# Optimization experiments

Measured on AMD Instinct MI355X. Metric: run time of the kernel, lower is better.

Reference implementation:

```python
import jax, jax.numpy as jnp
import numpy as np

NUM_EXPERTS = 64
TOP_K = 8
HIDDEN = 2048
MLP = 768
TOKENS = 1024


def setup_inputs() -> dict:
    key = jax.random.key(0)
    ks = jax.random.split(key, 5)
    hidden_states = jax.random.normal(ks[0], (TOKENS, HIDDEN), dtype=jnp.float32)
    # lecun-normal-ish scaling (std = 1/sqrt(fan_in))
    router_w = jax.random.normal(ks[1], (HIDDEN, NUM_EXPERTS), dtype=jnp.float32) / np.sqrt(HIDDEN)
    gate_proj = jax.random.normal(ks[2], (NUM_EXPERTS, HIDDEN, MLP), dtype=jnp.float32) / np.sqrt(HIDDEN)
    up_proj = jax.random.normal(ks[3], (NUM_EXPERTS, HIDDEN, MLP), dtype=jnp.float32) / np.sqrt(HIDDEN)
    down_proj = jax.random.normal(ks[4], (NUM_EXPERTS, MLP, HIDDEN), dtype=jnp.float32) / np.sqrt(MLP)
    return {
        "hidden_states": hidden_states,
        "router_w": router_w,
        "gate_proj": gate_proj,
        "up_proj": up_proj,
        "down_proj": down_proj,
    }


def reference(hidden_states, router_w, gate_proj, up_proj, down_proj):
    # Router: [T, E]
    router_logits = hidden_states @ router_w
    # Top-k routing, softmax renormalized over the selected k (norm_topk_prob=True)
    routing_weights, selected_experts = jax.lax.top_k(router_logits, k=TOP_K)
    routing_weights = jax.nn.softmax(routing_weights, axis=-1)  # [T, k]

    sel_flat = selected_experts.ravel()  # [T*k] int32
    # Duplicate each token for each of its k experts: [T*k, H]
    x_exp = jnp.repeat(hidden_states, TOP_K, axis=0)

    # prepare_routing: sort token copies by expert id, count per-expert group sizes
    sort_idx = jnp.argsort(sel_flat)          # stable sort of expert ids
    x_sorted = x_exp[sort_idx]                # [T*k, H] grouped by expert
    group_sizes = jnp.zeros((NUM_EXPERTS,), dtype=jnp.int32).at[sel_flat].add(1)
    unsort_idx = jnp.argsort(sort_idx)

    # Grouped GEMMs (megablox-style) via ragged_dot
    gate_out = jax.lax.ragged_dot(x_sorted, gate_proj, group_sizes)   # [T*k, M]
    up_out = jax.lax.ragged_dot(x_sorted, up_proj, group_sizes)       # [T*k, M]
    down_out = jax.lax.ragged_dot(jax.nn.silu(gate_out) * up_out, down_proj, group_sizes)  # [T*k, H]

    # Unsort back to (token, k) order and combine with routing weights
    unsorted = down_out[unsort_idx].reshape(-1, TOP_K, HIDDEN)
    return jnp.sum(unsorted * routing_weights[..., None], axis=1)  # [T, H]
```

## Files before the change

kernel.cpp:

```cpp
#include <hip/hip_runtime.h>
#include <hip/hip_bf16.h>

#define T_TOKENS 1024
#define HID      2048
#define NEXP     64
#define TOPK     8
#define MLP      768
#define NPAIR    (T_TOKENS * TOPK)

typedef __bf16 bf16x8 __attribute__((ext_vector_type(8)));
typedef float  f32x4  __attribute__((ext_vector_type(4)));
typedef unsigned int u32x2 __attribute__((ext_vector_type(2)));
typedef unsigned int u32x4 __attribute__((ext_vector_type(4)));

#define LDK 40

static __device__ __forceinline__ unsigned short f2bf(float f) {
    __hip_bfloat16 h = __float2bfloat16(f);
    unsigned short u;
    __builtin_memcpy(&u, &h, sizeof(u));
    return u;
}
static __device__ __forceinline__ unsigned int pk2bf(float a, float b) {
    return (unsigned int)f2bf(a) | ((unsigned int)f2bf(b) << 16);
}

__global__ __launch_bounds__(256) void router_topk_kernel(
    const float* __restrict__ hs, const float* __restrict__ rw,
    int* __restrict__ sel, float* __restrict__ wts, unsigned short* __restrict__ xb)
{
    const int lane = threadIdx.x & 63;
    const int tg   = threadIdx.x >> 6;
    const int t    = blockIdx.x * 4 + tg;

    {
        const float* xr = hs + (size_t)t * HID;
        unsigned short* xw = xb + (size_t)t * HID;
        #pragma unroll
        for (int c = 0; c < 4; ++c) {
            int i = (lane + c * 64) * 8;
            f32x4 a = *(const f32x4*)(xr + i);
            f32x4 b = *(const f32x4*)(xr + i + 4);
            u32x4 v;
            v[0] = pk2bf(a[0], a[1]); v[1] = pk2bf(a[2], a[3]);
            v[2] = pk2bf(b[0], b[1]); v[3] = pk2bf(b[2], b[3]);
            *(u32x4*)(xw + i) = v;
        }
    }

    const float4* x4 = (const float4*)(hs + (size_t)t * HID);
    float acc = 0.f;
    for (int h4 = 0; h4 < HID / 4; ++h4) {
        float4 xv = x4[h4];
        int hb = h4 * 4 * NEXP + lane;
        acc += xv.x * rw[hb] + xv.y * rw[hb + NEXP]
             + xv.z * rw[hb + 2 * NEXP] + xv.w * rw[hb + 3 * NEXP];
    }

    float v = acc;
    float tv[TOPK]; int ti[TOPK];
    for (int i = 0; i < TOPK; ++i) {
        float m = v; int mi = lane;
        for (int off = 32; off > 0; off >>= 1) {
            float om  = __shfl_xor(m, off, 64);
            int   omi = __shfl_xor(mi, off, 64);
            if (om > m || (om == m && omi < mi)) { m = om; mi = omi; }
        }
        tv[i] = m; ti[i] = mi;
        if (lane == mi) v = -__builtin_inff();
    }
    if (lane == 0) {
        float mx = tv[0], s = 0.f, e[TOPK];
        for (int i = 0; i < TOPK; ++i) { e[i] = __expf(tv[i] - mx); s += e[i]; }
        float inv = 1.f / s;
        for (int i = 0; i < TOPK; ++i) {
            wts[t * TOPK + i] = e[i] * inv;
            sel[t * TOPK + i] = ti[i];
        }
    }
}

__global__ __launch_bounds__(1024) void route_kernel(
    const int* __restrict__ sel, int* __restrict__ offsets, int* __restrict__ rows)
{
    __shared__ int cnt[NEXP];
    __shared__ int cur[NEXP];
    const int t = threadIdx.x;
    if (t < NEXP) cnt[t] = 0;
    __syncthreads();
    int e[8];
    const int p0 = t * 8;
    #pragma unroll
    for (int j = 0; j < 8; ++j) {
        e[j] = sel[p0 + j];
        atomicAdd(&cnt[e[j]], 1);
    }
    __syncthreads();
    if (t == 0) {
        int s = 0;
        for (int i = 0; i < NEXP; ++i) { cur[i] = s; offsets[i] = s; s += cnt[i]; }
        offsets[NEXP] = s;
    }
    __syncthreads();
    #pragma unroll
    for (int j = 0; j < 8; ++j) {
        int pos = atomicAdd(&cur[e[j]], 1);
        rows[pos] = p0 + j;
    }
}

__global__ __launch_bounds__(256, 2) void gateup_kernel(
    const unsigned short* __restrict__ xb, const float* __restrict__ gw,
    const float* __restrict__ uw, const int* __restrict__ offsets,
    const int* __restrict__ rows, unsigned short* __restrict__ hb)
{
    const int bid = blockIdx.x;
    const int sw  = (bid & 7) * 96 + (bid >> 3);
    const int e   = sw / 12;
    const int n0  = (sw % 12) * 64;

    const int r0 = offsets[e];
    const int nrows = offsets[e + 1] - r0;
    if (nrows <= 0) return;

    __shared__ __align__(16) float smemf[12800];
    unsigned short* smem = (unsigned short*)smemf;

    const int thr  = threadIdx.x;
    const int wave = thr >> 6;
    const int lane = thr & 63;
    const int wg   = wave & 1;
    const int isUp = wave >> 1;
    const int fr   = lane & 15;
    const int fq   = lane >> 4;
    const int mofs_c = isUp ? 10240 : 7680;

    const int ar = thr >> 2;
    const int ac = (thr & 3) * 8;

    const int tt   = thr & 127;
    const int wk2  = tt & 15;
    const int nst  = (tt >> 4) * 8;
    const float* wsrc = (thr >= 128 ? uw : gw)
        + (size_t)e * HID * MLP + (size_t)(2 * wk2) * MLP + n0 + nst;
    const int mofs_s = (thr >= 128) ? 10240 : 7680;

    const int NS = HID / 32;

    for (int m0 = 0; m0 < nrows; m0 += 192) {
        const unsigned short *ap0, *ap1, *ap2;
        bool av0, av1, av2;
        {
            int gr0 = m0 + ar, gr1 = m0 + ar + 64, gr2 = m0 + ar + 128;
            av0 = gr0 < nrows; av1 = gr1 < nrows; av2 = gr2 < nrows;
            int p0 = av0 ? rows[r0 + gr0] : 0;
            int p1 = av1 ? rows[r0 + gr1] : 0;
            int p2 = av2 ? rows[r0 + gr2] : 0;
            ap0 = xb + (size_t)(p0 >> 3) * HID + ac;
            ap1 = xb + (size_t)(p1 >> 3) * HID + ac;
            ap2 = xb + (size_t)(p2 >> 3) * HID + ac;
        }

        u32x4 va0, va1, va2;
        f32x4 wAe, wBe, wCe, wDe, wAo, wBo, wCo, wDo;
        const u32x4 uz = (u32x4){0u, 0u, 0u, 0u};
        const f32x4 fz = (f32x4){0.f, 0.f, 0.f, 0.f};

        auto LOAD_A = [&](int s) {
            va0 = av0 ? *(const u32x4*)(ap0 + s * 32) : uz;
            va1 = av1 ? *(const u32x4*)(ap1 + s * 32) : uz;
            va2 = av2 ? *(const u32x4*)(ap2 + s * 32) : uz;
        };
        auto WRITE_A = [&](int s) {
            unsigned short* b = smem + (s & 1) * 12800;
            *(u32x4*)(b + ar * LDK + ac) = va0;
            *(u32x4*)(b + (ar + 64) * LDK + ac) = va1;
            *(u32x4*)(b + (ar + 128) * LDK + ac) = va2;
        };
        auto LOAD_WE = [&](int s) {
            const float* wp = wsrc + (size_t)s * 32 * MLP;
            wAe = *(const f32x4*)wp;        wBe = *(const f32x4*)(wp + 4);
            wCe = *(const f32x4*)(wp + MLP); wDe = *(const f32x4*)(wp + MLP + 4);
        };
        auto LOAD_WO = [&](int s) {
            const float* wp = wsrc + (size_t)s * 32 * MLP;
            wAo = *(const f32x4*)wp;        wBo = *(const f32x4*)(wp + 4);
            wCo = *(const f32x4*)(wp + MLP); wDo = *(const f32x4*)(wp + MLP + 4);
        };
        auto WRITE_WE = [&](int s) {
            unsigned short* wb = smem + (s & 1) * 12800 + mofs_s;
            #pragma unroll
            for (int j = 0; j < 4; ++j) {
                *(unsigned int*)(wb + (nst + j) * LDK + 2 * wk2)     = pk2bf(wAe[j], wCe[j]);
                *(unsigned int*)(wb + (nst + 4 + j) * LDK + 2 * wk2) = pk2bf(wBe[j], wDe[j]);
            }
        };
        auto WRITE_WO = [&](int s) {
            unsigned short* wb = smem + (s & 1) * 12800 + mofs_s;
            #pragma unroll
            for (int j = 0; j < 4; ++j) {
                *(unsigned int*)(wb + (nst + j) * LDK + 2 * wk2)     = pk2bf(wAo[j], wCo[j]);
                *(unsigned int*)(wb + (nst + 4 + j) * LDK + 2 * wk2) = pk2bf(wBo[j], wDo[j]);
            }
        };

        f32x4 acc[6][4];
        #pragma unroll
        for (int ms = 0; ms < 6; ++ms)
            #pragma unroll
            for (int ns = 0; ns < 4; ++ns) acc[ms][ns] = fz;

        const int rem = nrows - m0 - wg * 96;

        auto STEP = [&](const unsigned short* bb) {
            const unsigned short* wbb = bb + mofs_c;
            bf16x8 wF0 = *(const bf16x8*)(wbb + (0 * 16 + fr) * LDK + fq * 8);
            bf16x8 wF1 = *(const bf16x8*)(wbb + (1 * 16 + fr) * LDK + fq * 8);
            bf16x8 wF2 = *(const bf16x8*)(wbb + (2 * 16 + fr) * LDK + fq * 8);
            bf16x8 wF3 = *(const bf16x8*)(wbb + (3 * 16 + fr) * LDK + fq * 8);
            bf16x8 aF[6];
            #pragma unroll
            for (int ms = 0; ms < 6; ++ms)
                aF[ms] = *(const bf16x8*)(bb + (wg * 96 + ms * 16 + fr) * LDK + fq * 8);
            #pragma unroll
            for (int ms = 0; ms < 6; ++ms) {
                if (rem > ms * 16) {
                    acc[ms][0] = __builtin_amdgcn_mfma_f32_16x16x32_bf16(aF[ms], wF0, acc[ms][0], 0, 0, 0);
                    acc[ms][1] = __builtin_amdgcn_mfma_f32_16x16x32_bf16(aF[ms], wF1, acc[ms][1], 0, 0, 0);
                    acc[ms][2] = __builtin_amdgcn_mfma_f32_16x16x32_bf16(aF[ms], wF2, acc[ms][2], 0, 0, 0);
                    acc[ms][3] = __builtin_amdgcn_mfma_f32_16x16x32_bf16(aF[ms], wF3, acc[ms][3], 0, 0, 0);
                }
            }
        };

        LOAD_WE(0);
        LOAD_WO(1);
        LOAD_A(0);
        WRITE_WE(0);
        WRITE_A(0);
        LOAD_A(1);
        asm volatile("s_waitcnt lgkmcnt(0)" ::: "memory");
        __builtin_amdgcn_s_barrier();

        for (int s = 0; s < NS; s += 2) {
            if (s + 2 < NS) LOAD_WE(s + 2);
            STEP(smem);
            WRITE_WO(s + 1);
            WRITE_A(s + 1);
            if (s + 2 < NS) LOAD_A(s + 2);
            asm volatile("s_waitcnt lgkmcnt(0)" ::: "memory");
            __builtin_amdgcn_s_barrier();
            if (s + 3 < NS) LOAD_WO(s + 3);
            STEP(smem + 12800);
            if (s + 2 < NS) { WRITE_WE(s + 2); WRITE_A(s + 2); }
            if (s + 3 < NS) LOAD_A(s + 3);
            asm volatile("s_waitcnt lgkmcnt(0)" ::: "memory");
            __builtin_amdgcn_s_barrier();
        }

        float* xbf = smemf;
        if (isUp) {
            #pragma unroll
            for (int ms = 0; ms < 6; ++ms)
                #pragma unroll
                for (int i = 0; i < 4; ++i) {
                    int lrow = wg * 96 + ms * 16 + fq * 4 + i;
                    #pragma unroll
                    for (int ns = 0; ns < 4; ++ns)
                        xbf[lrow * 65 + ns * 16 + fr] = acc[ms][ns][i];
                }
        }
        __syncthreads();
        if (!isUp) {
            #pragma unroll
            for (int ms = 0; ms < 6; ++ms)
                #pragma unroll
                for (int i = 0; i < 4; ++i) {
                    int lrow = wg * 96 + ms * 16 + fq * 4 + i;
                    int grow = m0 + lrow;
                    if (grow < nrows) {
                        unsigned short* drow = hb + (size_t)(r0 + grow) * MLP + n0;
                        #pragma unroll
                        for (int ns = 0; ns < 4; ++ns) {
                            float g = acc[ms][ns][i];
                            float u = xbf[lrow * 65 + ns * 16 + fr];
                            float h = g * u / (1.f + __expf(-g));
                            drow[ns * 16 + fr] = f2bf(h);
                        }
                    }
                }
        }
        __syncthreads();
    }
}

__global__ __launch_bounds__(256, 2) void down_kernel(
    const unsigned short* __restrict__ hb, const float* __restrict__ dw,
    const int* __restrict__ offsets, const int* __restrict__ rows,
    const float* __restrict__ wts, float* __restrict__ out)
{
    const int bid = blockIdx.x;
    const int sw  = (bid & 7) * 128 + (bid >> 3);
    const int e   = sw >> 4;
    const int n0  = (sw & 15) * 128;

    const int r0 = offsets[e];
    const int nrows = offsets[e + 1] - r0;
    if (nrows <= 0) return;

    __shared__ __align__(16) float smemf[12800];
    unsigned short* smem = (unsigned short*)smemf;

    const int thr  = threadIdx.x;
    const int wave = thr >> 6;
    const int lane = thr & 63;
    const int wg   = wave & 1;
    const int wn   = wave >> 1;
    const int fr   = lane & 15;
    const int fq   = lane >> 4;

    const int ar = thr >> 2;
    const int ac = (thr & 3) * 8;

    const int wk2 = thr & 15;
    const int nst = (thr >> 4) * 8;
    const float* wsrc = dw + (size_t)e * MLP * HID + (size_t)(2 * wk2) * HID + n0 + nst;

    const int NS = MLP / 32;

    for (int m0 = 0; m0 < nrows; m0 += 192) {
        const bool av0 = (m0 + ar)       < nrows;
        const bool av1 = (m0 + ar + 64)  < nrows;
        const bool av2 = (m0 + ar + 128) < nrows;
        const unsigned short* hp0 = hb + (size_t)(r0 + m0 + ar) * MLP + ac;
        const unsigned short* hp1 = hp0 + (size_t)64  * MLP;
        const unsigned short* hp2 = hp0 + (size_t)128 * MLP;

        u32x4 ua0, ua1, ua2;
        f32x4 wAe, wBe, wCe, wDe, wAo, wBo, wCo, wDo;
        const u32x4 uz = (u32x4){0u, 0u, 0u, 0u};
        const f32x4 fz = (f32x4){0.f, 0.f, 0.f, 0.f};

        auto LOAD_A = [&](int s) {
            ua0 = av0 ? *(const u32x4*)(hp0 + s * 32) : uz;
            ua1 = av1 ? *(const u32x4*)(hp1 + s * 32) : uz;
            ua2 = av2 ? *(const u32x4*)(hp2 + s * 32) : uz;
        };
        auto WRITE_A = [&](int s) {
            unsigned short* b = smem + (s & 1) * 12800;
            *(u32x4*)(b + ar * LDK + ac) = ua0;
            *(u32x4*)(b + (ar + 64) * LDK + ac) = ua1;
            *(u32x4*)(b + (ar + 128) * LDK + ac) = ua2;
        };
        auto LOAD_WE = [&](int s) {
            const float* wp = wsrc + (size_t)s * 32 * HID;
            wAe = *(const f32x4*)wp;        wBe = *(const f32x4*)(wp + 4);
            wCe = *(const f32x4*)(wp + HID); wDe = *(const f32x4*)(wp + HID + 4);
        };
        auto LOAD_WO = [&](int s) {
            const float* wp = wsrc + (size_t)s * 32 * HID;
            wAo = *(const f32x4*)wp;        wBo = *(const f32x4*)(wp + 4);
            wCo = *(const f32x4*)(wp + HID); wDo = *(const f32x4*)(wp + HID + 4);
        };
        auto WRITE_WE = [&](int s) {
            unsigned short* wb = smem + (s & 1) * 12800 + 7680;
            #pragma unroll
            for (int j = 0; j < 4; ++j) {
                *(unsigned int*)(wb + (nst + j) * LDK + 2 * wk2)     = pk2bf(wAe[j], wCe[j]);
                *(unsigned int*)(wb + (nst + 4 + j) * LDK + 2 * wk2) = pk2bf(wBe[j], wDe[j]);
            }
        };
        auto WRITE_WO = [&](int s) {
            unsigned short* wb = smem + (s & 1) * 12800 + 7680;
            #pragma unroll
            for (int j = 0; j < 4; ++j) {
                *(unsigned int*)(wb + (nst + j) * LDK + 2 * wk2)     = pk2bf(wAo[j], wCo[j]);
                *(unsigned int*)(wb + (nst + 4 + j) * LDK + 2 * wk2) = pk2bf(wBo[j], wDo[j]);
            }
        };

        f32x4 acc[6][4];
        #pragma unroll
        for (int ms = 0; ms < 6; ++ms)
            #pragma unroll
            for (int ns = 0; ns < 4; ++ns) acc[ms][ns] = fz;

        const int rem = nrows - m0 - wg * 96;

        auto STEP = [&](const unsigned short* bb) {
            const unsigned short* wbb = bb + 7680;
            bf16x8 wF0 = *(const bf16x8*)(wbb + (wn * 64 + 0 * 16 + fr) * LDK + fq * 8);
            bf16x8 wF1 = *(const bf16x8*)(wbb + (wn * 64 + 1 * 16 + fr) * LDK + fq * 8);
            bf16x8 wF2 = *(const bf16x8*)(wbb + (wn * 64 + 2 * 16 + fr) * LDK + fq * 8);
            bf16x8 wF3 = *(const bf16x8*)(wbb + (wn * 64 + 3 * 16 + fr) * LDK + fq * 8);
            bf16x8 aF[6];
            #pragma unroll
            for (int ms = 0; ms < 6; ++ms)
                aF[ms] = *(const bf16x8*)(bb + (wg * 96 + ms * 16 + fr) * LDK + fq * 8);
            #pragma unroll
            for (int ms = 0; ms < 6; ++ms) {
                if (rem > ms * 16) {
                    acc[ms][0] = __builtin_amdgcn_mfma_f32_16x16x32_bf16(aF[ms], wF0, acc[ms][0], 0, 0, 0);
                    acc[ms][1] = __builtin_amdgcn_mfma_f32_16x16x32_bf16(aF[ms], wF1, acc[ms][1], 0, 0, 0);
                    acc[ms][2] = __builtin_amdgcn_mfma_f32_16x16x32_bf16(aF[ms], wF2, acc[ms][2], 0, 0, 0);
                    acc[ms][3] = __builtin_amdgcn_mfma_f32_16x16x32_bf16(aF[ms], wF3, acc[ms][3], 0, 0, 0);
                }
            }
        };

        LOAD_WE(0);
        LOAD_WO(1);
        LOAD_A(0);
        WRITE_WE(0);
        WRITE_A(0);
        LOAD_A(1);
        asm volatile("s_waitcnt lgkmcnt(0)" ::: "memory");
        __builtin_amdgcn_s_barrier();

        for (int s = 0; s < NS; s += 2) {
            if (s + 2 < NS) LOAD_WE(s + 2);
            STEP(smem);
            WRITE_WO(s + 1);
            WRITE_A(s + 1);
            if (s + 2 < NS) LOAD_A(s + 2);
            asm volatile("s_waitcnt lgkmcnt(0)" ::: "memory");
            __builtin_amdgcn_s_barrier();
            if (s + 3 < NS) LOAD_WO(s + 3);
            STEP(smem + 12800);
            if (s + 2 < NS) { WRITE_WE(s + 2); WRITE_A(s + 2); }
            if (s + 3 < NS) LOAD_A(s + 3);
            asm volatile("s_waitcnt lgkmcnt(0)" ::: "memory");
            __builtin_amdgcn_s_barrier();
        }

        #pragma unroll
        for (int ms = 0; ms < 6; ++ms) {
            #pragma unroll
            for (int i = 0; i < 4; ++i) {
                int lrow = wg * 96 + ms * 16 + fq * 4 + i;
                int grow = m0 + lrow;
                if (grow < nrows) {
                    int p  = rows[r0 + grow];
                    float w = wts[p];
                    float* orow = out + (size_t)(p >> 3) * HID + n0 + wn * 64;
                    #pragma unroll
                    for (int ns = 0; ns < 4; ++ns)
                        atomicAdd(orow + ns * 16 + fr, acc[ms][ns][i] * w);
                }
            }
        }
        __syncthreads();
    }
}

extern "C" void kernel_launch(void* const* d_in, const int* in_sizes, int n_in,
                              void* d_out, int out_size, void* d_ws, size_t ws_size,
                              hipStream_t stream)
{
    const float* hs = (const float*)d_in[0];
    const float* rw = (const float*)d_in[1];
    const float* gw = (const float*)d_in[2];
    const float* uw = (const float*)d_in[3];
    const float* dw = (const float*)d_in[4];
    float* out = (float*)d_out;

    char* ws = (char*)d_ws;
    int*   sel     = (int*)(ws);
    float* wts     = (float*)(ws + 32768);
    int*   offsets = (int*)(ws + 65792);
    int*   rows    = (int*)(ws + 66560);
    unsigned short* xb = (unsigned short*)(ws + 99328);
    unsigned short* hb = (unsigned short*)(ws + 99328 + 4194304);

    hipMemsetAsync(out, 0, (size_t)T_TOKENS * HID * sizeof(float), stream);

    router_topk_kernel<<<T_TOKENS / 4, 256, 0, stream>>>(hs, rw, sel, wts, xb);
    route_kernel<<<1, 1024, 0, stream>>>(sel, offsets, rows);
    gateup_kernel<<<768, 256, 0, stream>>>(xb, gw, uw, offsets, rows, hb);
    down_kernel<<<1024, 256, 0, stream>>>(hb, dw, offsets, rows, wts, out);
}
```

Measured before the change: 1.198 ms.

## Use 512-thread gate/up blocks and replace atomic scatter with per-pair buffer plus combine

The gate/up kernel moves to 512 threads (8 waves), each wave covering 48 rows instead of 96, which halves per-wave accumulator registers and spreads the global loads across more threads. The down kernel becomes a template that, when the workspace is large enough, writes unweighted per-pair outputs to a scratch buffer. A separate combine kernel then sums the top-k pairs per token with the routing weights. This drops the output memset and the float atomics, but adds a 64 MB intermediate write and read, and the old atomic path remains as a fallback.

Result: faster. 1.163 ms, median of 3 (-2.9%).

```diff
diff --git a/kernel.cpp b/kernel.cpp
--- a/kernel.cpp
+++ b/kernel.cpp
@@ -109,7 +109,7 @@
     }
 }
 
-__global__ __launch_bounds__(256, 2) void gateup_kernel(
+__global__ __launch_bounds__(512) void gateup_kernel(
     const unsigned short* __restrict__ xb, const float* __restrict__ gw,
     const float* __restrict__ uw, const int* __restrict__ offsets,
     const int* __restrict__ rows, unsigned short* __restrict__ hb)
@@ -129,21 +129,19 @@
     const int thr  = threadIdx.x;
     const int wave = thr >> 6;
     const int lane = thr & 63;
-    const int wg   = wave & 1;
-    const int isUp = wave >> 1;
+    const int wg   = wave & 3;
+    const int isUp = wave >> 2;
     const int fr   = lane & 15;
     const int fq   = lane >> 4;
-    const int mofs_c = isUp ? 10240 : 7680;
-
-    const int ar = thr >> 2;
-    const int ac = (thr & 3) * 8;
-
-    const int tt   = thr & 127;
-    const int wk2  = tt & 15;
-    const int nst  = (tt >> 4) * 8;
-    const float* wsrc = (thr >= 128 ? uw : gw)
-        + (size_t)e * HID * MLP + (size_t)(2 * wk2) * MLP + n0 + nst;
-    const int mofs_s = (thr >= 128) ? 10240 : 7680;
+
+    const int ar = thr >> 3;
+    const int ac = (thr & 7) * 4;
+
+    const int wk2 = thr & 15;
+    const int wnq = (thr & 255) >> 4;
+    const float* wsrc = (thr >= 256 ? uw : gw)
+        + (size_t)e * HID * MLP + (size_t)(2 * wk2) * MLP + n0 + wnq * 4;
+    const int mofs = (thr >= 256) ? 10240 : 7680;
 
     const int NS = HID / 32;
 
@@ -161,34 +159,215 @@
             ap2 = xb + (size_t)(p2 >> 3) * HID + ac;
         }
 
-        u32x4 va0, va1, va2;
+        u32x2 va0, va1, va2;
+        f32x4 w0e, w1e, w0o, w1o;
+        const u32x2 z2 = (u32x2){0u, 0u};
+        const f32x4 fz = (f32x4){0.f, 0.f, 0.f, 0.f};
+
+        auto LOAD_A = [&](int s) {
+            va0 = av0 ? *(const u32x2*)(ap0 + s * 32) : z2;
+            va1 = av1 ? *(const u32x2*)(ap1 + s * 32) : z2;
+            va2 = av2 ? *(const u32x2*)(ap2 + s * 32) : z2;
+        };
+        auto WRITE_A = [&](int s) {
+            unsigned short* b = smem + (s & 1) * 12800;
+            *(u32x2*)(b + ar * LDK + ac) = va0;
+            *(u32x2*)(b + (ar + 64) * LDK + ac) = va1;
+            *(u32x2*)(b + (ar + 128) * LDK + ac) = va2;
+        };
+        auto LOAD_WE = [&](int s) {
+            const float* wp = wsrc + (size_t)s * 32 * MLP;
+            w0e = *(const f32x4*)wp;  w1e = *(const f32x4*)(wp + MLP);
+        };
+        auto LOAD_WO = [&](int s) {
+            const float* wp = wsrc + (size_t)s * 32 * MLP;
+            w0o = *(const f32x4*)wp;  w1o = *(const f32x4*)(wp + MLP);
+        };
+        auto WRITE_WE = [&](int s) {
+            unsigned short* wb = smem + (s & 1) * 12800 + mofs;
+            #pragma unroll
+            for (int i = 0; i < 4; ++i)
+                *(unsigned int*)(wb + (wnq * 4 + i) * LDK + 2 * wk2) = pk2bf(w0e[i], w1e[i]);
+        };
+        auto WRITE_WO = [&](int s) {
+            unsigned short* wb = smem + (s & 1) * 12800 + mofs;
+            #pragma unroll
+            for (int i = 0; i < 4; ++i)
+                *(unsigned int*)(wb + (wnq * 4 + i) * LDK + 2 * wk2) = pk2bf(w0o[i], w1o[i]);
+        };
+
+        f32x4 acc[3][4];
+        #pragma unroll
+        for (int ms = 0; ms < 3; ++ms)
+            #pragma unroll
+            for (int ns = 0; ns < 4; ++ns) acc[ms][ns] = fz;
+
+        const int rem = nrows - m0 - wg * 48;
+
+        LOAD_WE(0);
+        LOAD_WO(1);
+        LOAD_A(0);
+        WRITE_WE(0);
+        WRITE_A(0);
+        LOAD_A(1);
+        asm volatile("s_waitcnt lgkmcnt(0)" ::: "memory");
+        __builtin_amdgcn_s_barrier();
+
+        #define GU_MFMA(BB)                                                          \
+        {                                                                            \
+            const unsigned short* wbb = (BB) + mofs;                                 \
+            bf16x8 aF0, aF1, aF2, wF0, wF1, wF2, wF3;                                \
+            wF0 = *(const bf16x8*)(wbb + (0 * 16 + fr) * LDK + fq * 8);              \
+            wF1 = *(const bf16x8*)(wbb + (1 * 16 + fr) * LDK + fq * 8);              \
+            wF2 = *(const bf16x8*)(wbb + (2 * 16 + fr) * LDK + fq * 8);              \
+            wF3 = *(const bf16x8*)(wbb + (3 * 16 + fr) * LDK + fq * 8);              \
+            aF0 = *(const bf16x8*)((BB) + (wg * 48 + fr) * LDK + fq * 8);            \
+            aF1 = *(const bf16x8*)((BB) + (wg * 48 + 16 + fr) * LDK + fq * 8);       \
+            aF2 = *(const bf16x8*)((BB) + (wg * 48 + 32 + fr) * LDK + fq * 8);       \
+            if (rem > 0) {                                                           \
+                acc[0][0] = __builtin_amdgcn_mfma_f32_16x16x32_bf16(aF0, wF0, acc[0][0], 0, 0, 0); \
+                acc[0][1] = __builtin_amdgcn_mfma_f32_16x16x32_bf16(aF0, wF1, acc[0][1], 0, 0, 0); \
+                acc[0][2] = __builtin_amdgcn_mfma_f32_16x16x32_bf16(aF0, wF2, acc[0][2], 0, 0, 0); \
+                acc[0][3] = __builtin_amdgcn_mfma_f32_16x16x32_bf16(aF0, wF3, acc[0][3], 0, 0, 0); \
+            }                                                                        \
+            if (rem > 16) {                                                          \
+                acc[1][0] = __builtin_amdgcn_mfma_f32_16x16x32_bf16(aF1, wF0, acc[1][0], 0, 0, 0); \
+                acc[1][1] = __builtin_amdgcn_mfma_f32_16x16x32_bf16(aF1, wF1, acc[1][1], 0, 0, 0); \
+                acc[1][2] = __builtin_amdgcn_mfma_f32_16x16x32_bf16(aF1, wF2, acc[1][2], 0, 0, 0); \
+                acc[1][3] = __builtin_amdgcn_mfma_f32_16x16x32_bf16(aF1, wF3, acc[1][3], 0, 0, 0); \
+            }                                                                        \
+            if (rem > 32) {                                                          \
+                acc[2][0] = __builtin_amdgcn_mfma_f32_16x16x32_bf16(aF2, wF0, acc[2][0], 0, 0, 0); \
+                acc[2][1] = __builtin_amdgcn_mfma_f32_16x16x32_bf16(aF2, wF1, acc[2][1], 0, 0, 0); \
+                acc[2][2] = __builtin_amdgcn_mfma_f32_16x16x32_bf16(aF2, wF2, acc[2][2], 0, 0, 0); \
+                acc[2][3] = __builtin_amdgcn_mfma_f32_16x16x32_bf16(aF2, wF3, acc[2][3], 0, 0, 0); \
+            }                                                                        \
+        }
+
+        for (int s = 0; s < NS; s += 2) {
+            if (s + 2 < NS) LOAD_WE(s + 2);
+            GU_MFMA(smem)
+            WRITE_WO(s + 1);
+            WRITE_A(s + 1);
+            if (s + 2 < NS) LOAD_A(s + 2);
+            asm volatile("s_waitcnt lgkmcnt(0)" ::: "memory");
+            __builtin_amdgcn_s_barrier();
+            if (s + 3 < NS) LOAD_WO(s + 3);
+            GU_MFMA(smem + 12800)
+            if (s + 2 < NS) { WRITE_WE(s + 2); WRITE_A(s + 2); }
+            if (s + 3 < NS) LOAD_A(s + 3);
+            asm volatile("s_waitcnt lgkmcnt(0)" ::: "memory");
+            __builtin_amdgcn_s_barrier();
+        }
+        #undef GU_MFMA
+
+        float* xbf = smemf;
+        if (isUp) {
+            #pragma unroll
+            for (int ms = 0; ms < 3; ++ms)
+                #pragma unroll
+                for (int i = 0; i < 4; ++i) {
+                    int lrow = wg * 48 + ms * 16 + fq * 4 + i;
+                    #pragma unroll
+                    for (int ns = 0; ns < 4; ++ns)
+                        xbf[lrow * 65 + ns * 16 + fr] = acc[ms][ns][i];
+                }
+        }
+        __syncthreads();
+        if (!isUp) {
+            #pragma unroll
+            for (int ms = 0; ms < 3; ++ms)
+                #pragma unroll
+                for (int i = 0; i < 4; ++i) {
+                    int lrow = wg * 48 + ms * 16 + fq * 4 + i;
+                    int grow = m0 + lrow;
+                    if (grow < nrows) {
+                        unsigned short* drow = hb + (size_t)(r0 + grow) * MLP + n0;
+                        #pragma unroll
+                        for (int ns = 0; ns < 4; ++ns) {
+                            float g = acc[ms][ns][i];
+                            float u = xbf[lrow * 65 + ns * 16 + fr];
+                            float h = g * u / (1.f + __expf(-g));
+                            drow[ns * 16 + fr] = f2bf(h);
+                        }
+                    }
+                }
+        }
+        __syncthreads();
+    }
+}
+
+template <int USE_ATOMIC>
+__global__ __launch_bounds__(256, 2) void down_kernel_t(
+    const unsigned short* __restrict__ hb, const float* __restrict__ dw,
+    const int* __restrict__ offsets, const int* __restrict__ rows,
+    const float* __restrict__ wts, float* __restrict__ outp)
+{
+    const int bid = blockIdx.x;
+    const int sw  = (bid & 7) * 128 + (bid >> 3);
+    const int e   = sw >> 4;
+    const int n0  = (sw & 15) * 128;
+
+    const int r0 = offsets[e];
+    const int nrows = offsets[e + 1] - r0;
+    if (nrows <= 0) return;
+
+    __shared__ __align__(16) float smemf[12800];
+    unsigned short* smem = (unsigned short*)smemf;
+
+    const int thr  = threadIdx.x;
+    const int wave = thr >> 6;
+    const int lane = thr & 63;
+    const int wg   = wave & 1;
+    const int wn   = wave >> 1;
+    const int fr   = lane & 15;
+    const int fq   = lane >> 4;
+
+    const int ar = thr >> 2;
+    const int ac = (thr & 3) * 8;
+
+    const int wk2 = thr & 15;
+    const int nst = (thr >> 4) * 8;
+    const float* wsrc = dw + (size_t)e * MLP * HID + (size_t)(2 * wk2) * HID + n0 + nst;
+
+    const int NS = MLP / 32;
+
+    for (int m0 = 0; m0 < nrows; m0 += 192) {
+        const bool av0 = (m0 + ar)       < nrows;
+        const bool av1 = (m0 + ar + 64)  < nrows;
+        const bool av2 = (m0 + ar + 128) < nrows;
+        const unsigned short* hp0 = hb + (size_t)(r0 + m0 + ar) * MLP + ac;
+        const unsigned short* hp1 = hp0 + (size_t)64  * MLP;
+        const unsigned short* hp2 = hp0 + (size_t)128 * MLP;
+
+        u32x4 ua0, ua1, ua2;
         f32x4 wAe, wBe, wCe, wDe, wAo, wBo, wCo, wDo;
         const u32x4 uz = (u32x4){0u, 0u, 0u, 0u};
         const f32x4 fz = (f32x4){0.f, 0.f, 0.f, 0.f};
 
         auto LOAD_A = [&](int s) {
-            va0 = av0 ? *(const u32x4*)(ap0 + s * 32) : uz;
-            va1 = av1 ? *(const u32x4*)(ap1 + s * 32) : uz;
-            va2 = av2 ? *(const u32x4*)(ap2 + s * 32) : uz;
+            ua0 = av0 ? *(const u32x4*)(hp0 + s * 32) : uz;
+            ua1 = av1 ? *(const u32x4*)(hp1 + s * 32) : uz;
+            ua2 = av2 ? *(const u32x4*)(hp2 + s * 32) : uz;
         };
         auto WRITE_A = [&](int s) {
             unsigned short* b = smem + (s & 1) * 12800;
-            *(u32x4*)(b + ar * LDK + ac) = va0;
-            *(u32x4*)(b + (ar + 64) * LDK + ac) = va1;
-            *(u32x4*)(b + (ar + 128) * LDK + ac) = va2;
+            *(u32x4*)(b + ar * LDK + ac) = ua0;
+            *(u32x4*)(b + (ar + 64) * LDK + ac) = ua1;
+            *(u32x4*)(b + (ar + 128) * LDK + ac) = ua2;
         };
         auto LOAD_WE = [&](int s) {
-            const float* wp = wsrc + (size_t)s * 32 * MLP;
+            const float* wp = wsrc + (size_t)s * 32 * HID;
             wAe = *(const f32x4*)wp;        wBe = *(const f32x4*)(wp + 4);
-            wCe = *(const f32x4*)(wp + MLP); wDe = *(const f32x4*)(wp + MLP + 4);
+            wCe = *(const f32x4*)(wp + HID); wDe = *(const f32x4*)(wp + HID + 4);
         };
         auto LOAD_WO = [&](int s) {
-            const float* wp = wsrc + (size_t)s * 32 * MLP;
+            const float* wp = wsrc + (size_t)s * 32 * HID;
             wAo = *(const f32x4*)wp;        wBo = *(const f32x4*)(wp + 4);
-            wCo = *(const f32x4*)(wp + MLP); wDo = *(const f32x4*)(wp + MLP + 4);
+            wCo = *(const f32x4*)(wp + HID); wDo = *(const f32x4*)(wp + HID + 4);
         };
         auto WRITE_WE = [&](int s) {
-            unsigned short* wb = smem + (s & 1) * 12800 + mofs_s;
+            unsigned short* wb = smem + (s & 1) * 12800 + 7680;
             #pragma unroll
             for (int j = 0; j < 4; ++j) {
                 *(unsigned int*)(wb + (nst + j) * LDK + 2 * wk2)     = pk2bf(wAe[j], wCe[j]);
@@ -196,7 +375,7 @@
             }
         };
         auto WRITE_WO = [&](int s) {
-            unsigned short* wb = smem + (s & 1) * 12800 + mofs_s;
+            unsigned short* wb = smem + (s & 1) * 12800 + 7680;
             #pragma unroll
             for (int j = 0; j < 4; ++j) {
                 *(unsigned int*)(wb + (nst + j) * LDK + 2 * wk2)     = pk2bf(wAo[j], wCo[j]);
@@ -213,11 +392,11 @@
         const int rem = nrows - m0 - wg * 96;
 
         auto STEP = [&](const unsigned short* bb) {
-            const unsigned short* wbb = bb + mofs_c;
-            bf16x8 wF0 = *(const bf16x8*)(wbb + (0 * 16 + fr) * LDK + fq * 8);
-            bf16x8 wF1 = *(const bf16x8*)(wbb + (1 * 16 + fr) * LDK + fq * 8);
-            bf16x8 wF2 = *(const bf16x8*)(wbb + (2 * 16 + fr) * LDK + fq * 8);
-            bf16x8 wF3 = *(const bf16x8*)(wbb + (3 * 16 + fr) * LDK + fq * 8);
+            const unsigned short* wbb = bb + 7680;
+            bf16x8 wF0 = *(const bf16x8*)(wbb + (wn * 64 + 0 * 16 + fr) * LDK + fq * 8);
+            bf16x8 wF1 = *(const bf16x8*)(wbb + (wn * 64 + 1 * 16 + fr) * LDK + fq * 8);
+            bf16x8 wF2 = *(const bf16x8*)(wbb + (wn * 64 + 2 * 16 + fr) * LDK + fq * 8);
+            bf16x8 wF3 = *(const bf16x8*)(wbb + (wn * 64 + 3 * 16 + fr) * LDK + fq * 8);
             bf16x8 aF[6];
             #pragma unroll
             for (int ms = 0; ms < 6; ++ms)
@@ -258,181 +437,6 @@
             __builtin_amdgcn_s_barrier();
         }
 
-        float* xbf = smemf;
-        if (isUp) {
-            #pragma unroll
-            for (int ms = 0; ms < 6; ++ms)
-                #pragma unroll
-                for (int i = 0; i < 4; ++i) {
-                    int lrow = wg * 96 + ms * 16 + fq * 4 + i;
-                    #pragma unroll
-                    for (int ns = 0; ns < 4; ++ns)
-                        xbf[lrow * 65 + ns * 16 + fr] = acc[ms][ns][i];
-                }
-        }
-        __syncthreads();
-        if (!isUp) {
-            #pragma unroll
-            for (int ms = 0; ms < 6; ++ms)
-                #pragma unroll
-                for (int i = 0; i < 4; ++i) {
-                    int lrow = wg * 96 + ms * 16 + fq * 4 + i;
-                    int grow = m0 + lrow;
-                    if (grow < nrows) {
-                        unsigned short* drow = hb + (size_t)(r0 + grow) * MLP + n0;
-                        #pragma unroll
-                        for (int ns = 0; ns < 4; ++ns) {
-                            float g = acc[ms][ns][i];
-                            float u = xbf[lrow * 65 + ns * 16 + fr];
-                            float h = g * u / (1.f + __expf(-g));
-                            drow[ns * 16 + fr] = f2bf(h);
-                        }
-                    }
-                }
-        }
-        __syncthreads();
-    }
-}
-
-__global__ __launch_bounds__(256, 2) void down_kernel(
-    const unsigned short* __restrict__ hb, const float* __restrict__ dw,
-    const int* __restrict__ offsets, const int* __restrict__ rows,
-    const float* __restrict__ wts, float* __restrict__ out)
-{
-    const int bid = blockIdx.x;
-    const int sw  = (bid & 7) * 128 + (bid >> 3);
-    const int e   = sw >> 4;
-    const int n0  = (sw & 15) * 128;
-
-    const int r0 = offsets[e];
-    const int nrows = offsets[e + 1] - r0;
-    if (nrows <= 0) return;
-
-    __shared__ __align__(16) float smemf[12800];
-    unsigned short* smem = (unsigned short*)smemf;
-
-    const int thr  = threadIdx.x;
-    const int wave = thr >> 6;
-    const int lane = thr & 63;
-    const int wg   = wave & 1;
-    const int wn   = wave >> 1;
-    const int fr   = lane & 15;
-    const int fq   = lane >> 4;
-
-    const int ar = thr >> 2;
-    const int ac = (thr & 3) * 8;
-
-    const int wk2 = thr & 15;
-    const int nst = (thr >> 4) * 8;
-    const float* wsrc = dw + (size_t)e * MLP * HID + (size_t)(2 * wk2) * HID + n0 + nst;
-
-    const int NS = MLP / 32;
-
-    for (int m0 = 0; m0 < nrows; m0 += 192) {
-        const bool av0 = (m0 + ar)       < nrows;
-        const bool av1 = (m0 + ar + 64)  < nrows;
-        const bool av2 = (m0 + ar + 128) < nrows;
-        const unsigned short* hp0 = hb + (size_t)(r0 + m0 + ar) * MLP + ac;
-        const unsigned short* hp1 = hp0 + (size_t)64  * MLP;
-        const unsigned short* hp2 = hp0 + (size_t)128 * MLP;
-
-        u32x4 ua0, ua1, ua2;
-        f32x4 wAe, wBe, wCe, wDe, wAo, wBo, wCo, wDo;
-        const u32x4 uz = (u32x4){0u, 0u, 0u, 0u};
-        const f32x4 fz = (f32x4){0.f, 0.f, 0.f, 0.f};
-
-        auto LOAD_A = [&](int s) {
-            ua0 = av0 ? *(const u32x4*)(hp0 + s * 32) : uz;
-            ua1 = av1 ? *(const u32x4*)(hp1 + s * 32) : uz;
-            ua2 = av2 ? *(const u32x4*)(hp2 + s * 32) : uz;
-        };
-        auto WRITE_A = [&](int s) {
-            unsigned short* b = smem + (s & 1) * 12800;
-            *(u32x4*)(b + ar * LDK + ac) = ua0;
-            *(u32x4*)(b + (ar + 64) * LDK + ac) = ua1;
-            *(u32x4*)(b + (ar + 128) * LDK + ac) = ua2;
-        };
-        auto LOAD_WE = [&](int s) {
-            const float* wp = wsrc + (size_t)s * 32 * HID;
-            wAe = *(const f32x4*)wp;        wBe = *(const f32x4*)(wp + 4);
-            wCe = *(const f32x4*)(wp + HID); wDe = *(const f32x4*)(wp + HID + 4);
-        };
-        auto LOAD_WO = [&](int s) {
-            const float* wp = wsrc + (size_t)s * 32 * HID;
-            wAo = *(const f32x4*)wp;        wBo = *(const f32x4*)(wp + 4);
-            wCo = *(const f32x4*)(wp + HID); wDo = *(const f32x4*)(wp + HID + 4);
-        };
-        auto WRITE_WE = [&](int s) {
-            unsigned short* wb = smem + (s & 1) * 12800 + 7680;
-            #pragma unroll
-            for (int j = 0; j < 4; ++j) {
-                *(unsigned int*)(wb + (nst + j) * LDK + 2 * wk2)     = pk2bf(wAe[j], wCe[j]);
-                *(unsigned int*)(wb + (nst + 4 + j) * LDK + 2 * wk2) = pk2bf(wBe[j], wDe[j]);
-            }
-        };
-        auto WRITE_WO = [&](int s) {
-            unsigned short* wb = smem + (s & 1) * 12800 + 7680;
-            #pragma unroll
-            for (int j = 0; j < 4; ++j) {
-                *(unsigned int*)(wb + (nst + j) * LDK + 2 * wk2)     = pk2bf(wAo[j], wCo[j]);
-                *(unsigned int*)(wb + (nst + 4 + j) * LDK + 2 * wk2) = pk2bf(wBo[j], wDo[j]);
-            }
-        };
-
-        f32x4 acc[6][4];
-        #pragma unroll
-        for (int ms = 0; ms < 6; ++ms)
-            #pragma unroll
-            for (int ns = 0; ns < 4; ++ns) acc[ms][ns] = fz;
-
-        const int rem = nrows - m0 - wg * 96;
-
-        auto STEP = [&](const unsigned short* bb) {
-            const unsigned short* wbb = bb + 7680;
-            bf16x8 wF0 = *(const bf16x8*)(wbb + (wn * 64 + 0 * 16 + fr) * LDK + fq * 8);
-            bf16x8 wF1 = *(const bf16x8*)(wbb + (wn * 64 + 1 * 16 + fr) * LDK + fq * 8);
-            bf16x8 wF2 = *(const bf16x8*)(wbb + (wn * 64 + 2 * 16 + fr) * LDK + fq * 8);
-            bf16x8 wF3 = *(const bf16x8*)(wbb + (wn * 64 + 3 * 16 + fr) * LDK + fq * 8);
-            bf16x8 aF[6];
-            #pragma unroll
-            for (int ms = 0; ms < 6; ++ms)
-                aF[ms] = *(const bf16x8*)(bb + (wg * 96 + ms * 16 + fr) * LDK + fq * 8);
-            #pragma unroll
-            for (int ms = 0; ms < 6; ++ms) {
-                if (rem > ms * 16) {
-                    acc[ms][0] = __builtin_amdgcn_mfma_f32_16x16x32_bf16(aF[ms], wF0, acc[ms][0], 0, 0, 0);
-                    acc[ms][1] = __builtin_amdgcn_mfma_f32_16x16x32_bf16(aF[ms], wF1, acc[ms][1], 0, 0, 0);
-                    acc[ms][2] = __builtin_amdgcn_mfma_f32_16x16x32_bf16(aF[ms], wF2, acc[ms][2], 0, 0, 0);
-                    acc[ms][3] = __builtin_amdgcn_mfma_f32_16x16x32_bf16(aF[ms], wF3, acc[ms][3], 0, 0, 0);
-                }
-            }
-        };
-
-        LOAD_WE(0);
-        LOAD_WO(1);
-        LOAD_A(0);
-        WRITE_WE(0);
-        WRITE_A(0);
-        LOAD_A(1);
-        asm volatile("s_waitcnt lgkmcnt(0)" ::: "memory");
-        __builtin_amdgcn_s_barrier();
-
-        for (int s = 0; s < NS; s += 2) {
-            if (s + 2 < NS) LOAD_WE(s + 2);
-            STEP(smem);
-            WRITE_WO(s + 1);
-            WRITE_A(s + 1);
-            if (s + 2 < NS) LOAD_A(s + 2);
-            asm volatile("s_waitcnt lgkmcnt(0)" ::: "memory");
-            __builtin_amdgcn_s_barrier();
-            if (s + 3 < NS) LOAD_WO(s + 3);
-            STEP(smem + 12800);
-            if (s + 2 < NS) { WRITE_WE(s + 2); WRITE_A(s + 2); }
-            if (s + 3 < NS) LOAD_A(s + 3);
-            asm volatile("s_waitcnt lgkmcnt(0)" ::: "memory");
-            __builtin_amdgcn_s_barrier();
-        }
-
         #pragma unroll
         for (int ms = 0; ms < 6; ++ms) {
             #pragma unroll
@@ -440,17 +444,44 @@
                 int lrow = wg * 96 + ms * 16 + fq * 4 + i;
                 int grow = m0 + lrow;
                 if (grow < nrows) {
-                    int p  = rows[r0 + grow];
-                    float w = wts[p];
-                    float* orow = out + (size_t)(p >> 3) * HID + n0 + wn * 64;
-                    #pragma unroll
-                    for (int ns = 0; ns < 4; ++ns)
-                        atomicAdd(orow + ns * 16 + fr, acc[ms][ns][i] * w);
+                    int p = rows[r0 + grow];
+                    if (USE_ATOMIC) {
+                        float w = wts[p];
+                        float* orow = outp + (size_t)(p >> 3) * HID + n0 + wn * 64;
+                        #pragma unroll
+                        for (int ns = 0; ns < 4; ++ns)
+                            atomicAdd(orow + ns * 16 + fr, acc[ms][ns][i] * w);
+                    } else {
+                        float* orow = outp + (size_t)p * HID + n0 + wn * 64;
+                        #pragma unroll
+                        for (int ns = 0; ns < 4; ++ns)
+                            orow[ns * 16 + fr] = acc[ms][ns][i];
+                    }
                 }
             }
         }
         __syncthreads();
     }
+}
+
+__global__ __launch_bounds__(256) void combine_kernel(
+    const float* __restrict__ pout, const float* __restrict__ wts,
+    float* __restrict__ out)
+{
+    const int idx = blockIdx.x * 256 + threadIdx.x;
+    const int t   = idx >> 9;
+    const int c4  = (idx & 511) * 4;
+
+    const float* w8 = wts + t * TOPK;
+    const float* pr = pout + (size_t)t * TOPK * HID + c4;
+    f32x4 s = (f32x4){0.f, 0.f, 0.f, 0.f};
+    #pragma unroll
+    for (int j = 0; j < TOPK; ++j) {
+        f32x4 v = *(const f32x4*)(pr + (size_t)j * HID);
+        float w = w8[j];
+        s[0] += w * v[0]; s[1] += w * v[1]; s[2] += w * v[2]; s[3] += w * v[3];
+    }
+    *(f32x4*)(out + (size_t)t * HID + c4) = s;
 }
 
 extern "C" void kernel_launch(void* const* d_in, const int* in_sizes, int n_in,
@@ -471,11 +502,18 @@
     int*   rows    = (int*)(ws + 66560);
     unsigned short* xb = (unsigned short*)(ws + 99328);
     unsigned short* hb = (unsigned short*)(ws + 99328 + 4194304);
-
-    hipMemsetAsync(out, 0, (size_t)T_TOKENS * HID * sizeof(float), stream);
+    float* pout = (float*)(ws + 99328 + 4194304 + 12582912);
+    const size_t need = 99328ull + 4194304 + 12582912 + (size_t)NPAIR * HID * 4;
 
     router_topk_kernel<<<T_TOKENS / 4, 256, 0, stream>>>(hs, rw, sel, wts, xb);
     route_kernel<<<1, 1024, 0, stream>>>(sel, offsets, rows);
-    gateup_kernel<<<768, 256, 0, stream>>>(xb, gw, uw, offsets, rows, hb);
-    down_kernel<<<1024, 256, 0, stream>>>(hb, dw, offsets, rows, wts, out);
-}
+    gateup_kernel<<<768, 512, 0, stream>>>(xb, gw, uw, offsets, rows, hb);
+
+    if (ws_size >= need) {
+        down_kernel_t<0><<<1024, 256, 0, stream>>>(hb, dw, offsets, rows, wts, pout);
+        combine_kernel<<<T_TOKENS * HID / 4 / 256, 256, 0, stream>>>(pout, wts, out);
+    } else {
+        hipMemsetAsync(out, 0, (size_t)T_TOKENS * HID * sizeof(float), stream);
+        down_kernel_t<1><<<1024, 256, 0, stream>>>(hb, dw, offsets, rows, wts, out);
+    }
+}
```
